# Optimization experiments

Hardware: AMD Instinct MI355X
Metric: run time of the kernel (lower is better)

Reference implementation:

```python
import jax, jax.numpy as jnp
import numpy as np

B, Q, HID = 2, 1024, 2048
NH, NKV, HD = 32, 8, 64          # num heads, kv heads, head_dim (HID = NH*HD)
GROUPS = NH // NKV
KB_N, TOPK = 512, 100            # kb entries, top_k_kb
KB_MAX_TRAIN = 512               # kb_max_train_triples (kb_length_scaling=True)
ROPE_THETA = 10000.0


def rotate_half(x):
    x1, x2 = jnp.split(x, 2, axis=-1)
    return jnp.concatenate([-x2, x1], axis=-1)


def setup_inputs() -> dict:
    key = jax.random.key(0)
    ks = jax.random.split(key, 10)
    sc = 1.0 / np.sqrt(HID)
    hidden_states = jax.random.normal(ks[0], (B, Q, HID), jnp.float32)
    kb_kvs = jax.random.normal(ks[1], (B, KB_N, HID), jnp.float32)
    Wq = jax.random.normal(ks[2], (HID, NH * HD), jnp.float32) * sc
    Wk = jax.random.normal(ks[3], (HID, NKV * HD), jnp.float32) * sc
    Wv = jax.random.normal(ks[4], (HID, NKV * HD), jnp.float32) * sc
    Wo = jax.random.normal(ks[5], (NH * HD, HID), jnp.float32) * sc
    Wq_new = jax.random.normal(ks[6], (HID, NH * HD), jnp.float32) * sc
    Wkb_k = jax.random.normal(ks[7], (HID, NKV * HD), jnp.float32) * sc
    Wkb_v = jax.random.normal(ks[8], (HID, NKV * HD), jnp.float32) * sc
    # RoPE tables [Q, HD]
    inv_freq = 1.0 / (ROPE_THETA ** (jnp.arange(0, HD, 2, dtype=jnp.float32) / HD))
    t = jnp.arange(Q, dtype=jnp.float32)
    freqs = t[:, None] * inv_freq[None, :]
    emb = jnp.concatenate([freqs, freqs], axis=-1)
    cos, sin = jnp.cos(emb), jnp.sin(emb)
    position_ids = jnp.broadcast_to(jnp.arange(Q), (B, Q))
    # additive causal mask [B,1,Q,Q]
    i = jnp.arange(Q)
    causal = jnp.where(i[None, :] <= i[:, None], 0.0, -1e9).astype(jnp.float32)
    attention_mask = jnp.broadcast_to(causal[None, None], (B, 1, Q, Q))
    return dict(hidden_states=hidden_states, kb_kvs=kb_kvs, Wq=Wq, Wk=Wk, Wv=Wv,
                Wo=Wo, Wq_new=Wq_new, Wkb_k=Wkb_k, Wkb_v=Wkb_v, cos=cos, sin=sin,
                attention_mask=attention_mask, position_ids=position_ids)


def attention_fwd(hidden_states, kb_kvs, Wq, Wk, Wv, Wo, Wq_new, Wkb_k, Wkb_v,
                  cos, sin, attention_mask, position_ids):
    b, q_len, _ = hidden_states.shape
    q = (hidden_states @ Wq).reshape(b, q_len, NH, HD).transpose(0, 2, 1, 3)
    k = (hidden_states @ Wk).reshape(b, q_len, NKV, HD).transpose(0, 2, 1, 3)
    v = (hidden_states @ Wv).reshape(b, q_len, NKV, HD).transpose(0, 2, 1, 3)
    # RoPE
    c = cos[position_ids][:, None]  # [b,1,q,hd]
    s = sin[position_ids][:, None]
    q = q * c + rotate_half(q) * s
    k = k * c + rotate_half(k) * s
    # repeat_kv (GQA expansion)
    k = jnp.repeat(k, GROUPS, axis=1)
    v = jnp.repeat(v, GROUPS, axis=1)
    # KB branch (layer_idx=0, kb_layer_index=0 -> slice is full hidden dim)
    kb_k = (kb_kvs @ Wkb_k).reshape(b, KB_N, NKV, HD).transpose(0, 2, 1, 3)
    kb_v = (kb_kvs @ Wkb_v).reshape(b, KB_N, NKV, HD).transpose(0, 2, 1, 3)
    kb_k = jnp.repeat(kb_k, GROUPS, axis=1)
    kb_v = jnp.repeat(kb_v, GROUPS, axis=1)
    kb_q = (hidden_states @ Wq_new).reshape(b, q_len, NH, HD).transpose(0, 2, 1, 3)
    scale = 1.0 / jnp.sqrt(jnp.float32(HD))
    aw_kb = jnp.einsum('bhqd,bhkd->bhqk', kb_q, kb_k) * scale  # [b,nh,q,KB_N]
    # top-k KB entry selection (scores summed over heads and query positions)
    sel_scores = aw_kb.sum(axis=(1, 2))                        # [b,KB_N]
    _, top_idx = jax.lax.top_k(sel_scores, TOPK)               # [b,TOPK]
    kb_v = jnp.take_along_axis(kb_v, top_idx[:, None, :, None], axis=2)
    aw_kb = jnp.take_along_axis(aw_kb, top_idx[:, None, None, :], axis=3)
    # kb length scaling: log(max_train_triples) - log(current kb len)
    aw_kb = aw_kb + (jnp.log(jnp.float32(KB_MAX_TRAIN)) - jnp.log(jnp.float32(TOPK)))
    aw_p = jnp.einsum('bhqd,bhkd->bhqk', q, k) * scale + attention_mask
    aw = jax.nn.softmax(jnp.concatenate([aw_kb, aw_p], axis=-1).astype(jnp.float32), axis=-1)
    aw = aw.astype(q.dtype)
    cv = jnp.concatenate([kb_v, v], axis=2)                    # [b,nh,TOPK+q,hd]
    out = jnp.einsum('bhqk,bhkd->bhqd', aw, cv)
    out = out.transpose(0, 2, 1, 3).reshape(b, q_len, NH * HD)
    return out @ Wo


def reference(hidden_states, kb_kvs, Wq, Wk, Wv, Wo, Wq_new, Wkb_k, Wkb_v,
              cos, sin, attention_mask, position_ids):
    return attention_fwd(hidden_states, kb_kvs, Wq, Wk, Wv, Wo, Wq_new, Wkb_k,
                         Wkb_v, cos, sin, attention_mask, position_ids)
```

## Files before the change

kernel.cpp:

```cpp
#include <hip/hip_runtime.h>

typedef unsigned short u16;
typedef unsigned int   u32;
typedef __bf16 bf16_t;
typedef bf16_t bf16x8 __attribute__((ext_vector_type(8)));
typedef float  floatx4 __attribute__((ext_vector_type(4)));

#define B_    2
#define QS    1024
#define HID_  2048
#define NH_   32
#define NKV_  8
#define HD_   64
#define KBN_  512
#define TOPK_ 100
#define FS    5120

__device__ __forceinline__ float b2f(u16 u) {
  union { u32 i; float f; } x; x.i = ((u32)u) << 16; return x.f;
}
__device__ __forceinline__ u16 f2b(float f) {
  union { float f; u32 i; } x; x.f = f;
  u32 r = x.i + 0x7fffu + ((x.i >> 16) & 1u);
  return (u16)(r >> 16);
}
__device__ __forceinline__ void async16(const u16* g, u16* l) {
  __builtin_amdgcn_global_load_lds(
      (const __attribute__((address_space(1))) unsigned int*)g,
      (__attribute__((address_space(3))) unsigned int*)l, 16, 0, 0);
}

__global__ __launch_bounds__(256)
void cast_f2b(const float* __restrict__ x, u16* __restrict__ y, int n4) {
  int i = blockIdx.x * 256 + threadIdx.x;
  if (i >= n4) return;
  float4 v = ((const float4*)x)[i];
  ((uint2*)y)[i] = make_uint2((u32)f2b(v.x) | ((u32)f2b(v.y) << 16),
                              (u32)f2b(v.z) | ((u32)f2b(v.w) << 16));
}

__global__ __launch_bounds__(256)
void transpose_cast_k(const float* __restrict__ W, u16* __restrict__ WT, int K, int N) {
  __shared__ float tile[32][33];
  int n0 = blockIdx.x * 32, k0 = blockIdx.y * 32;
  int tx = threadIdx.x & 31, ty = threadIdx.x >> 5;
#pragma unroll
  for (int i = 0; i < 32; i += 8)
    tile[ty + i][tx] = W[(size_t)(k0 + ty + i) * N + n0 + tx];
  __syncthreads();
#pragma unroll
  for (int i = 0; i < 32; i += 8)
    WT[(size_t)(n0 + ty + i) * K + k0 + tx] = f2b(tile[tx][ty + i]);
}

__global__ __launch_bounds__(512, 2)
void gemm256(const u16* __restrict__ A, const u16* __restrict__ BT,
             u16* __restrict__ C, int M, int N, int K, int CS) {
  (void)M;
  __shared__ __align__(16) u16 sm[65536];
  const int tid = threadIdx.x, lane = tid & 63, w = tid >> 6;
  const int wr = w >> 2, wc = w & 3;
  const int nbx = N >> 8;
  int nwg = gridDim.x, orig = blockIdx.x, swz = orig;
  if ((nwg & 7) == 0) swz = (orig & 7) * (nwg >> 3) + (orig >> 3);
  int bx = swz % nbx, by = swz / nbx;
  int m0 = by << 8, n0 = bx << 8;
  const int NT = K >> 6;

  int lr = lane >> 2;
  int colsw = ((lane & 3) * 8) ^ ((lane & 32) ? 16 : 0);
  const u16* gA[2][2]; const u16* gB[2][2];
  int lA[2][2];
#pragma unroll
  for (int h = 0; h < 2; ++h)
#pragma unroll
    for (int j = 0; j < 2; ++j) {
      int ij = 2 * w + j, kk = ij >> 3, rb = (ij & 7) * 16;
      gA[h][j] = A + (size_t)(m0 + h * 128 + rb + lr) * K + kk * 32 + colsw;
      gB[h][j] = BT + (size_t)(n0 + h * 128 + rb + lr) * K + kk * 32 + colsw;
      lA[h][j] = kk * 8192 + (h * 128 + rb) * 32;
    }
  int fsw = ((lane >> 4) * 8) ^ ((lane & 8) ? 16 : 0);
  int aoff = (wr * 128 + (lane & 15)) * 32 + fsw;
  int boff = 16384 + (wc * 64 + (lane & 15)) * 32 + fsw;

  floatx4 acc[8][4];
#pragma unroll
  for (int i = 0; i < 8; ++i)
#pragma unroll
    for (int j = 0; j < 4; ++j) acc[i][j] = (floatx4){0.f, 0.f, 0.f, 0.f};
  bf16x8 a[4][2], b[4][2];

#define STG_(g, l, u) async16((g) + (size_t)(u) * 64, &sm[(((u) & 1) << 15) + (l)])
#define BAR_ do { asm volatile("" ::: "memory"); __builtin_amdgcn_s_barrier(); \
                  asm volatile("" ::: "memory"); } while (0)
#define LG0_ do { asm volatile("s_waitcnt lgkmcnt(0)" ::: "memory"); \
                  __builtin_amdgcn_sched_barrier(0); } while (0)

  STG_(gA[0][0], lA[0][0], 0); STG_(gA[0][1], lA[0][1], 0);
  STG_(gA[1][0], lA[1][0], 0); STG_(gA[1][1], lA[1][1], 0);
  STG_(gB[0][0], lA[0][0] + 16384, 0); STG_(gB[0][1], lA[0][1] + 16384, 0);
  STG_(gB[1][0], lA[1][0] + 16384, 0); STG_(gB[1][1], lA[1][1] + 16384, 0);
  if (NT > 1) {
    STG_(gB[0][0], lA[0][0] + 16384, 1); STG_(gB[0][1], lA[0][1] + 16384, 1);
    STG_(gA[0][0], lA[0][0], 1); STG_(gA[0][1], lA[0][1], 1);
    asm volatile("s_waitcnt vmcnt(4)" ::: "memory");
  } else {
    asm volatile("s_waitcnt vmcnt(0)" ::: "memory");
  }
  BAR_;

  for (int u = 0; u < NT; ++u) {
    const int cb = (u & 1) << 15;
#pragma unroll
    for (int kk = 0; kk < 2; ++kk) {
#pragma unroll
      for (int mi = 0; mi < 4; ++mi)
        a[mi][kk] = *(const bf16x8*)&sm[cb + kk * 8192 + aoff + mi * 512];
#pragma unroll
      for (int ni = 0; ni < 2; ++ni)
        b[ni][kk] = *(const bf16x8*)&sm[cb + kk * 8192 + boff + ni * 512];
    }
    if (u + 1 < NT) { STG_(gA[1][0], lA[1][0], u + 1); STG_(gA[1][1], lA[1][1], u + 1); }
    BAR_; LG0_;
    __builtin_amdgcn_s_setprio(1);
#pragma unroll
    for (int mi = 0; mi < 4; ++mi)
#pragma unroll
      for (int ni = 0; ni < 2; ++ni)
#pragma unroll
        for (int kk = 0; kk < 2; ++kk)
          acc[mi][ni] = __builtin_amdgcn_mfma_f32_16x16x32_bf16(
              a[mi][kk], b[ni][kk], acc[mi][ni], 0, 0, 0);
    __builtin_amdgcn_s_setprio(0);
    BAR_;
#pragma unroll
    for (int kk = 0; kk < 2; ++kk)
#pragma unroll
      for (int ni = 0; ni < 2; ++ni)
        b[2 + ni][kk] = *(const bf16x8*)&sm[cb + kk * 8192 + boff + (2 + ni) * 512];
    if (u + 1 < NT) { STG_(gB[1][0], lA[1][0] + 16384, u + 1);
                      STG_(gB[1][1], lA[1][1] + 16384, u + 1); }
    BAR_; LG0_;
    __builtin_amdgcn_s_setprio(1);
#pragma unroll
    for (int mi = 0; mi < 4; ++mi)
#pragma unroll
      for (int ni = 0; ni < 2; ++ni)
#pragma unroll
        for (int kk = 0; kk < 2; ++kk)
          acc[mi][2 + ni] = __builtin_amdgcn_mfma_f32_16x16x32_bf16(
              a[mi][kk], b[2 + ni][kk], acc[mi][2 + ni], 0, 0, 0);
    __builtin_amdgcn_s_setprio(0);
    BAR_;
#pragma unroll
    for (int kk = 0; kk < 2; ++kk)
#pragma unroll
      for (int mi = 0; mi < 4; ++mi)
        a[mi][kk] = *(const bf16x8*)&sm[cb + kk * 8192 + aoff + 2048 + mi * 512];
    if (u + 2 < NT) { STG_(gB[0][0], lA[0][0] + 16384, u + 2);
                      STG_(gB[0][1], lA[0][1] + 16384, u + 2); }
    BAR_; LG0_;
    __builtin_amdgcn_s_setprio(1);
#pragma unroll
    for (int mi = 0; mi < 4; ++mi)
#pragma unroll
      for (int ni = 0; ni < 2; ++ni)
#pragma unroll
        for (int kk = 0; kk < 2; ++kk)
          acc[4 + mi][2 + ni] = __builtin_amdgcn_mfma_f32_16x16x32_bf16(
              a[mi][kk], b[2 + ni][kk], acc[4 + mi][2 + ni], 0, 0, 0);
    __builtin_amdgcn_s_setprio(0);
    BAR_;
    if (u + 2 < NT) {
      STG_(gA[0][0], lA[0][0], u + 2); STG_(gA[0][1], lA[0][1], u + 2);
      asm volatile("s_waitcnt vmcnt(4)" ::: "memory");
    } else {
      asm volatile("s_waitcnt vmcnt(0)" ::: "memory");
    }
    BAR_;
    __builtin_amdgcn_s_setprio(1);
#pragma unroll
    for (int mi = 0; mi < 4; ++mi)
#pragma unroll
      for (int ni = 0; ni < 2; ++ni)
#pragma unroll
        for (int kk = 0; kk < 2; ++kk)
          acc[4 + mi][ni] = __builtin_amdgcn_mfma_f32_16x16x32_bf16(
              a[mi][kk], b[ni][kk], acc[4 + mi][ni], 0, 0, 0);
    __builtin_amdgcn_s_setprio(0);
    BAR_;
  }
#undef STG_
#undef BAR_
#undef LG0_
  int quad = lane >> 4, col = lane & 15;
#pragma unroll
  for (int mi = 0; mi < 8; ++mi)
#pragma unroll
    for (int ni = 0; ni < 4; ++ni)
#pragma unroll
      for (int rr = 0; rr < 4; ++rr)
        C[(size_t)(m0 + wr * 128 + mi * 16 + quad * 4 + rr) * CS +
          n0 + wc * 64 + ni * 16 + col] = f2b(acc[mi][ni][rr]);
}

__global__ __launch_bounds__(512, 2)
void gemm256s(const u16* __restrict__ A, const u16* __restrict__ BT,
              float* __restrict__ P, int N, int LDK, int Kl, int ntiles) {
  __shared__ __align__(16) u16 sm[65536];
  const int tid = threadIdx.x, lane = tid & 63, w = tid >> 6;
  const int wr = w >> 2, wc = w & 3;
  const int nbx = N >> 8;
  int nwg = gridDim.x, orig = blockIdx.x, swz = orig;
  if ((nwg & 7) == 0) swz = (orig & 7) * (nwg >> 3) + (orig >> 3);
  int tile = swz % ntiles, slice = swz / ntiles;
  int bx = tile % nbx, by = tile / nbx;
  int m0 = by << 8, n0 = bx << 8;
  const int NT = Kl >> 6;
  const u16* As = A + (size_t)slice * Kl;
  const u16* Bs = BT + (size_t)slice * Kl;

  int lr = lane >> 2;
  int colsw = ((lane & 3) * 8) ^ ((lane & 32) ? 16 : 0);
  const u16* gA[2][2]; const u16* gB[2][2];
  int lA[2][2];
#pragma unroll
  for (int h = 0; h < 2; ++h)
#pragma unroll
    for (int j = 0; j < 2; ++j) {
      int ij = 2 * w + j, kk = ij >> 3, rb = (ij & 7) * 16;
      gA[h][j] = As + (size_t)(m0 + h * 128 + rb + lr) * LDK + kk * 32 + colsw;
      gB[h][j] = Bs + (size_t)(n0 + h * 128 + rb + lr) * LDK + kk * 32 + colsw;
      lA[h][j] = kk * 8192 + (h * 128 + rb) * 32;
    }
  int fsw = ((lane >> 4) * 8) ^ ((lane & 8) ? 16 : 0);
  int aoff = (wr * 128 + (lane & 15)) * 32 + fsw;
  int boff = 16384 + (wc * 64 + (lane & 15)) * 32 + fsw;

  floatx4 acc[8][4];
#pragma unroll
  for (int i = 0; i < 8; ++i)
#pragma unroll
    for (int j = 0; j < 4; ++j) acc[i][j] = (floatx4){0.f, 0.f, 0.f, 0.f};
  bf16x8 a[4][2], b[4][2];

#define STG_(g, l, u) async16((g) + (size_t)(u) * 64, &sm[(((u) & 1) << 15) + (l)])
#define BAR_ do { asm volatile("" ::: "memory"); __builtin_amdgcn_s_barrier(); \
                  asm volatile("" ::: "memory"); } while (0)
#define LG0_ do { asm volatile("s_waitcnt lgkmcnt(0)" ::: "memory"); \
                  __builtin_amdgcn_sched_barrier(0); } while (0)

  STG_(gA[0][0], lA[0][0], 0); STG_(gA[0][1], lA[0][1], 0);
  STG_(gA[1][0], lA[1][0], 0); STG_(gA[1][1], lA[1][1], 0);
  STG_(gB[0][0], lA[0][0] + 16384, 0); STG_(gB[0][1], lA[0][1] + 16384, 0);
  STG_(gB[1][0], lA[1][0] + 16384, 0); STG_(gB[1][1], lA[1][1] + 16384, 0);
  if (NT > 1) {
    STG_(gB[0][0], lA[0][0] + 16384, 1); STG_(gB[0][1], lA[0][1] + 16384, 1);
    STG_(gA[0][0], lA[0][0], 1); STG_(gA[0][1], lA[0][1], 1);
    asm volatile("s_waitcnt vmcnt(4)" ::: "memory");
  } else {
    asm volatile("s_waitcnt vmcnt(0)" ::: "memory");
  }
  BAR_;

  for (int u = 0; u < NT; ++u) {
    const int cb = (u & 1) << 15;
#pragma unroll
    for (int kk = 0; kk < 2; ++kk) {
#pragma unroll
      for (int mi = 0; mi < 4; ++mi)
        a[mi][kk] = *(const bf16x8*)&sm[cb + kk * 8192 + aoff + mi * 512];
#pragma unroll
      for (int ni = 0; ni < 2; ++ni)
        b[ni][kk] = *(const bf16x8*)&sm[cb + kk * 8192 + boff + ni * 512];
    }
    if (u + 1 < NT) { STG_(gA[1][0], lA[1][0], u + 1); STG_(gA[1][1], lA[1][1], u + 1); }
    BAR_; LG0_;
    __builtin_amdgcn_s_setprio(1);
#pragma unroll
    for (int mi = 0; mi < 4; ++mi)
#pragma unroll
      for (int ni = 0; ni < 2; ++ni)
#pragma unroll
        for (int kk = 0; kk < 2; ++kk)
          acc[mi][ni] = __builtin_amdgcn_mfma_f32_16x16x32_bf16(
              a[mi][kk], b[ni][kk], acc[mi][ni], 0, 0, 0);
    __builtin_amdgcn_s_setprio(0);
    BAR_;
#pragma unroll
    for (int kk = 0; kk < 2; ++kk)
#pragma unroll
      for (int ni = 0; ni < 2; ++ni)
        b[2 + ni][kk] = *(const bf16x8*)&sm[cb + kk * 8192 + boff + (2 + ni) * 512];
    if (u + 1 < NT) { STG_(gB[1][0], lA[1][0] + 16384, u + 1);
                      STG_(gB[1][1], lA[1][1] + 16384, u + 1); }
    BAR_; LG0_;
    __builtin_amdgcn_s_setprio(1);
#pragma unroll
    for (int mi = 0; mi < 4; ++mi)
#pragma unroll
      for (int ni = 0; ni < 2; ++ni)
#pragma unroll
        for (int kk = 0; kk < 2; ++kk)
          acc[mi][2 + ni] = __builtin_amdgcn_mfma_f32_16x16x32_bf16(
              a[mi][kk], b[2 + ni][kk], acc[mi][2 + ni], 0, 0, 0);
    __builtin_amdgcn_s_setprio(0);
    BAR_;
#pragma unroll
    for (int kk = 0; kk < 2; ++kk)
#pragma unroll
      for (int mi = 0; mi < 4; ++mi)
        a[mi][kk] = *(const bf16x8*)&sm[cb + kk * 8192 + aoff + 2048 + mi * 512];
    if (u + 2 < NT) { STG_(gB[0][0], lA[0][0] + 16384, u + 2);
                      STG_(gB[0][1], lA[0][1] + 16384, u + 2); }
    BAR_; LG0_;
    __builtin_amdgcn_s_setprio(1);
#pragma unroll
    for (int mi = 0; mi < 4; ++mi)
#pragma unroll
      for (int ni = 0; ni < 2; ++ni)
#pragma unroll
        for (int kk = 0; kk < 2; ++kk)
          acc[4 + mi][2 + ni] = __builtin_amdgcn_mfma_f32_16x16x32_bf16(
              a[mi][kk], b[2 + ni][kk], acc[4 + mi][2 + ni], 0, 0, 0);
    __builtin_amdgcn_s_setprio(0);
    BAR_;
    if (u + 2 < NT) {
      STG_(gA[0][0], lA[0][0], u + 2); STG_(gA[0][1], lA[0][1], u + 2);
      asm volatile("s_waitcnt vmcnt(4)" ::: "memory");
    } else {
      asm volatile("s_waitcnt vmcnt(0)" ::: "memory");
    }
    BAR_;
    __builtin_amdgcn_s_setprio(1);
#pragma unroll
    for (int mi = 0; mi < 4; ++mi)
#pragma unroll
      for (int ni = 0; ni < 2; ++ni)
#pragma unroll
        for (int kk = 0; kk < 2; ++kk)
          acc[4 + mi][ni] = __builtin_amdgcn_mfma_f32_16x16x32_bf16(
              a[mi][kk], b[ni][kk], acc[4 + mi][ni], 0, 0, 0);
    __builtin_amdgcn_s_setprio(0);
    BAR_;
  }
#undef STG_
#undef BAR_
#undef LG0_
  int quad = lane >> 4, col = lane & 15;
  float* Pp = P + (size_t)slice * ((size_t)ntiles << 16);
#pragma unroll
  for (int mi = 0; mi < 8; ++mi)
#pragma unroll
    for (int ni = 0; ni < 4; ++ni)
#pragma unroll
      for (int rr = 0; rr < 4; ++rr)
        Pp[(size_t)(m0 + wr * 128 + mi * 16 + quad * 4 + rr) * N +
           n0 + wc * 64 + ni * 16 + col] = acc[mi][ni][rr];
}

template <bool TOB16>
__global__ __launch_bounds__(256)
void redp_k(const float* __restrict__ P, void* __restrict__ out, int nslice, int len4) {
  int i = blockIdx.x * 256 + threadIdx.x;
  if (i >= len4) return;
  float4 a = ((const float4*)P)[i];
  for (int s = 1; s < nslice; ++s) {
    float4 b = ((const float4*)P)[(size_t)s * len4 + i];
    a.x += b.x; a.y += b.y; a.z += b.z; a.w += b.w;
  }
  if constexpr (TOB16)
    ((uint2*)out)[i] = make_uint2((u32)f2b(a.x) | ((u32)f2b(a.y) << 16),
                                  (u32)f2b(a.z) | ((u32)f2b(a.w) << 16));
  else
    ((float4*)out)[i] = a;
}

__global__ __launch_bounds__(256)
void rope_k(u16* __restrict__ x, int rs, const float* __restrict__ ct,
            const float* __restrict__ st, const int* __restrict__ pid, int nh, int total) {
  int gid = blockIdx.x * 256 + threadIdx.x;
  if (gid >= total) return;
  int per_row = nh * 32;
  int row = gid / per_row;
  int rem = gid - row * per_row;
  int h = rem >> 5, d = rem & 31;
  int pos = pid[row];
  float c = ct[pos * 64 + d];
  float s = st[pos * 64 + d];
  size_t base = (size_t)row * rs + h * 64 + d;
  float x0 = b2f(x[base]), x1 = b2f(x[base + 32]);
  x[base]      = f2b(x0 * c - x1 * s);
  x[base + 32] = f2b(x1 * c + x0 * s);
}

__global__ __launch_bounds__(256)
void red_d_k(const double* __restrict__ part, double* __restrict__ out, int nchunk, int len) {
  int i = blockIdx.x * 256 + threadIdx.x;
  if (i >= len) return;
  double a = 0.0;
  for (int c = 0; c < nchunk; ++c) a += part[(size_t)c * len + i];
  out[i] = a;
}

__global__ __launch_bounds__(256)
void hssum_part_k(const float* __restrict__ hs, double* __restrict__ part) {
  int qc = blockIdx.x, b = blockIdx.y, t = threadIdx.x;
  double a[8] = {0, 0, 0, 0, 0, 0, 0, 0};
  for (int qq = 0; qq < 16; ++qq) {
    const float* row = hs + (size_t)(b * QS + qc * 16 + qq) * HID_;
#pragma unroll
    for (int m = 0; m < 8; ++m) a[m] += (double)row[m * 256 + t];
  }
#pragma unroll
  for (int m = 0; m < 8; ++m)
    part[(size_t)qc * (B_ * HID_) + b * HID_ + m * 256 + t] = a[m];
}

__global__ __launch_bounds__(512)
void selS_part_k(const double* __restrict__ hssum, const float* __restrict__ Wqn,
                 double* __restrict__ part) {
  int chunk = blockIdx.x, b = blockIdx.y, j = threadIdx.x;
  int g = j >> 6, d = j & 63;
  int c0 = chunk * 16;
  double acc = 0.0;
  for (int cc = 0; cc < 16; ++cc) {
    int c = c0 + cc;
    const float* w = Wqn + (size_t)c * HID_ + g * 256 + d;
    acc += hssum[b * HID_ + c] *
           ((double)w[0] + (double)w[64] + (double)w[128] + (double)w[192]);
  }
  part[(size_t)chunk * (B_ * 512) + b * 512 + j] = acc;
}

__global__ __launch_bounds__(256)
void selU_part_k(const double* __restrict__ S, const float* __restrict__ Wkbk,
                 double* __restrict__ part) {
  int jc = blockIdx.x;
  int b = blockIdx.y >> 3;
  int c = (blockIdx.y & 7) * 256 + threadIdx.x;
  const float* row = Wkbk + (size_t)c * 512 + jc * 128;
  const double* Sp = S + b * 512 + jc * 128;
  double acc = 0.0;
  for (int j = 0; j < 128; j += 4) {
    float4 wv = *(const float4*)(row + j);
    acc += Sp[j] * (double)wv.x + Sp[j + 1] * (double)wv.y +
           Sp[j + 2] * (double)wv.z + Sp[j + 3] * (double)wv.w;
  }
  part[(size_t)jc * (B_ * HID_) + b * HID_ + c] = acc;
}

__global__ __launch_bounds__(256)
void self_part_k(const double* __restrict__ U, const float* __restrict__ kbin,
                 double* __restrict__ part) {
  int n = blockIdx.x * 256 + threadIdx.x;
  int cc = blockIdx.y, b = blockIdx.z;
  const float* row = kbin + (size_t)(b * KBN_ + n) * HID_ + cc * 256;
  const double* u = U + b * HID_ + cc * 256;
  double acc = 0.0;
  for (int c = 0; c < 256; c += 4) {
    float4 kv = *(const float4*)(row + c);
    acc += u[c] * (double)kv.x + u[c + 1] * (double)kv.y +
           u[c + 2] * (double)kv.z + u[c + 3] * (double)kv.w;
  }
  part[(size_t)cc * (B_ * KBN_) + b * KBN_ + n] = acc;
}

__global__ __launch_bounds__(512)
void topk_rank_k(const double* __restrict__ partSel, int* __restrict__ idx) {
  int b = blockIdx.x, i = threadIdx.x;
  __shared__ float v[KBN_];
  double a = 0.0;
#pragma unroll
  for (int c = 0; c < 8; ++c) a += partSel[(size_t)c * (B_ * KBN_) + b * KBN_ + i];
  float vi = (float)a;
  v[i] = vi;
  __syncthreads();
  int rank = 0;
#pragma unroll 8
  for (int j = 0; j < KBN_; ++j) {
    float vj = v[j];
    rank += (vj > vi || (vj == vi && j < i)) ? 1 : 0;
  }
  if (rank < TOPK_) idx[b * TOPK_ + rank] = i;
}

__global__ __launch_bounds__(256)
void vtrans_k(const u16* __restrict__ fused, u16* __restrict__ vt) {
  int kt = blockIdx.x;
  int bg = blockIdx.y;
  int b = bg >> 3, g = bg & 7;
  int t = threadIdx.x;
  __shared__ u16 tile[64][72];
  {
    int kk = t >> 2, dc = (t & 3) * 16;
    const u16* src = fused + (size_t)(b * QS + kt * 64 + kk) * FS + 2560 + g * 64 + dc;
    *(uint4*)&tile[kk][dc]     = *(const uint4*)src;
    *(uint4*)&tile[kk][dc + 8] = *(const uint4*)(src + 8);
  }
  __syncthreads();
  {
    int d = t >> 2, kc = t & 3;
    __align__(16) u16 tmp[16];
#pragma unroll
    for (int i = 0; i < 16; ++i) tmp[i] = tile[kc * 16 + i][d];
    u16* dst = vt + ((size_t)bg * 64 + d) * 1024 + kt * 64 + kc * 16;
    *(uint4*)dst       = *(uint4*)&tmp[0];
    *(uint4*)(dst + 8) = *(uint4*)&tmp[8];
  }
}

__global__ __launch_bounds__(256)
void kbgather_k(const u16* __restrict__ kbf, const int* __restrict__ topidx,
                u16* __restrict__ kbt) {
  int bg = blockIdx.x; int b = bg >> 3, g = bg & 7;
  int t = threadIdx.x;
  int d = t >> 2, s0 = (t & 3) * 32;
  __align__(16) u16 tmp[32];
#pragma unroll
  for (int i = 0; i < 32; ++i) {
    int slot = s0 + i;
    int n = topidx[b * TOPK_ + (slot < TOPK_ ? slot : TOPK_ - 1)];
    tmp[i] = kbf[(size_t)(b * KBN_ + n) * 1024 + 512 + g * 64 + d];
  }
  u16* dst = kbt + ((size_t)bg * 64 + d) * 128 + s0;
#pragma unroll
  for (int i = 0; i < 32; i += 8) *(uint4*)(dst + i) = *(uint4*)&tmp[i];
}

__global__ __launch_bounds__(256)
void attn_mfma_k(const u16* __restrict__ fused, const u16* __restrict__ kbf,
                 const u16* __restrict__ vt, const u16* __restrict__ kbt,
                 const int* __restrict__ topidx, u16* __restrict__ ctx) {
  int bid = blockIdx.x;
  int raw = bid >> 6;
  int hb = bid & 63;
  int h = hb & 31, b = hb >> 5;
  int pg = raw >> 2, pp = raw & 3;
  int pbase = (pg >> 1) * 4 + pp;
  int qt = (pg & 1) ? (15 - pbase) : pbase;
  int g = h >> 2;
  int t = threadIdx.x, lane = t & 63, w = t >> 6;
  int quad = lane >> 4, col = lane & 15;
  __shared__ __align__(16) u16 ks[64 * 72];
  __shared__ __align__(16) u16 vst[64 * 64];
  __shared__ __align__(16) u16 ps[4][16 * 72];
  const float LOGADJ = 1.6331544f;
  int q0 = qt * 64;

  int qrow_frag = q0 + w * 16 + col;
  bf16x8 aKB[2], aC[2];
#pragma unroll
  for (int kstep = 0; kstep < 2; ++kstep) {
    const u16* p1 = fused + (size_t)(b * QS + qrow_frag) * FS + 3072 + h * 64 + kstep * 32 + quad * 8;
    const u16* p2 = fused + (size_t)(b * QS + qrow_frag) * FS + 0    + h * 64 + kstep * 32 + quad * 8;
    uint4 x1 = *(const uint4*)p1, x2 = *(const uint4*)p2;
    const u16* u1 = (const u16*)&x1; const u16* u2 = (const u16*)&x2;
#pragma unroll
    for (int i = 0; i < 8; ++i) {
      aKB[kstep][i] = (bf16_t)(0.125f * b2f(u1[i]));
      aC[kstep][i]  = (bf16_t)(0.125f * b2f(u2[i]));
    }
  }

  float mrow[4] = {-1e30f, -1e30f, -1e30f, -1e30f};
  float lrow[4] = {0.f, 0.f, 0.f, 0.f};
  floatx4 acc[4];
#pragma unroll
  for (int nb = 0; nb < 4; ++nb) acc[nb] = (floatx4){0.f, 0.f, 0.f, 0.f};

  int sj = t >> 2, sdc = (t & 3) * 16, sc4 = t & 3;
  uint4 kr0, kr1, vr0, vr1;

#define LOADTILE(TT) do {                                                      \
    int _t = (TT);                                                             \
    const u16 *_src, *_vsrc;                                                   \
    if (_t < 2) {                                                              \
      int _slot = _t * 64 + sj;                                                \
      int _n = topidx[b * TOPK_ + (_slot < TOPK_ ? _slot : TOPK_ - 1)];        \
      _src = kbf + (size_t)(b * KBN_ + _n) * 1024 + g * 64 + sdc;              \
      _vsrc = kbt + ((size_t)(b * 8 + g) * 64 + sj) * 128 + _t * 64 + sc4 * 16;\
    } else {                                                                   \
      int _key = (_t - 2) * 64 + sj;                                           \
      _src = fused + (size_t)(b * QS + _key) * FS + 2048 + g * 64 + sdc;       \
      _vsrc = vt + ((size_t)(b * 8 + g) * 64 + sj) * 1024 + (_t - 2) * 64 + sc4 * 16; \
    }                                                                          \
    kr0 = *(const uint4*)_src;  kr1 = *(const uint4*)(_src + 8);               \
    vr0 = *(const uint4*)_vsrc; vr1 = *(const uint4*)(_vsrc + 8);              \
  } while (0)

  int ntiles = 2 + (q0 >> 6) + 1;
  LOADTILE(0);
  for (int tile = 0; tile < ntiles; ++tile) {
    __syncthreads();
    *(uint4*)&ks[sj * 72 + sdc]     = kr0;
    *(uint4*)&ks[sj * 72 + sdc + 8] = kr1;
    {
      int sw = sj & 7;
      *(uint4*)&vst[sj * 64 + ((2 * sc4)     ^ sw) * 8] = vr0;
      *(uint4*)&vst[sj * 64 + ((2 * sc4 + 1) ^ sw) * 8] = vr1;
    }
    if (tile + 1 < ntiles) LOADTILE(tile + 1);
    __syncthreads();

    bf16x8 aq0 = (tile < 2) ? aKB[0] : aC[0];
    bf16x8 aq1 = (tile < 2) ? aKB[1] : aC[1];
    floatx4 s[4];
#pragma unroll
    for (int nb = 0; nb < 4; ++nb) {
      s[nb] = (floatx4){0.f, 0.f, 0.f, 0.f};
      bf16x8 b0 = *(bf16x8*)&ks[(nb * 16 + col) * 72 + quad * 8];
      bf16x8 b1 = *(bf16x8*)&ks[(nb * 16 + col) * 72 + 32 + quad * 8];
      s[nb] = __builtin_amdgcn_mfma_f32_16x16x32_bf16(aq0, b0, s[nb], 0, 0, 0);
      s[nb] = __builtin_amdgcn_mfma_f32_16x16x32_bf16(aq1, b1, s[nb], 0, 0, 0);
    }
    if (tile < 2) {
      if (tile == 0) {
#pragma unroll
        for (int nb = 0; nb < 4; ++nb)
#pragma unroll
          for (int rr = 0; rr < 4; ++rr) s[nb][rr] += LOGADJ;
      } else {
#pragma unroll
        for (int nb = 0; nb < 4; ++nb) {
          bool dead = (64 + nb * 16 + col) >= TOPK_;
#pragma unroll
          for (int rr = 0; rr < 4; ++rr)
            s[nb][rr] = dead ? -1e30f : (s[nb][rr] + LOGADJ);
        }
      }
    } else if (tile == ntiles - 1) {
      int kbase = (tile - 2) * 64;
#pragma unroll
      for (int nb = 0; nb < 4; ++nb) {
        int key = kbase + nb * 16 + col;
#pragma unroll
        for (int rr = 0; rr < 4; ++rr) {
          int qrow = q0 + w * 16 + quad * 4 + rr;
          if (key > qrow) s[nb][rr] = -1e30f;
        }
      }
    }
    float tm[4];
#pragma unroll
    for (int rr = 0; rr < 4; ++rr)
      tm[rr] = fmaxf(fmaxf(s[0][rr], s[1][rr]), fmaxf(s[2][rr], s[3][rr]));
#pragma unroll
    for (int off = 1; off < 16; off <<= 1)
#pragma unroll
      for (int rr = 0; rr < 4; ++rr)
        tm[rr] = fmaxf(tm[rr], __shfl_xor(tm[rr], off));
    float alpha[4], rs[4];
#pragma unroll
    for (int rr = 0; rr < 4; ++rr) {
      float mn = fmaxf(mrow[rr], tm[rr]);
      alpha[rr] = __expf(mrow[rr] - mn);
      mrow[rr] = mn;
      rs[rr] = 0.f;
    }
#pragma unroll
    for (int nb = 0; nb < 4; ++nb)
#pragma unroll
      for (int rr = 0; rr < 4; ++rr) {
        float ev = __expf(s[nb][rr] - mrow[rr]);
        rs[rr] += ev;
        ps[w][(quad * 4 + rr) * 72 + nb * 16 + col] = f2b(ev);
      }
#pragma unroll
    for (int off = 1; off < 16; off <<= 1)
#pragma unroll
      for (int rr = 0; rr < 4; ++rr)
        rs[rr] += __shfl_xor(rs[rr], off);
#pragma unroll
    for (int rr = 0; rr < 4; ++rr) lrow[rr] = lrow[rr] * alpha[rr] + rs[rr];
#pragma unroll
    for (int nb = 0; nb < 4; ++nb)
#pragma unroll
      for (int rr = 0; rr < 4; ++rr) acc[nb][rr] *= alpha[rr];

    bf16x8 pa0 = *(bf16x8*)&ps[w][col * 72 + quad * 8];
    bf16x8 pa1 = *(bf16x8*)&ps[w][col * 72 + 32 + quad * 8];
#pragma unroll
    for (int nb = 0; nb < 4; ++nb) {
      int d = nb * 16 + col;
      int sw = (d & 7) << 3;
      bf16x8 vb0 = *(bf16x8*)&vst[d * 64 + ((quad * 8) ^ sw)];
      bf16x8 vb1 = *(bf16x8*)&vst[d * 64 + ((32 + quad * 8) ^ sw)];
      acc[nb] = __builtin_amdgcn_mfma_f32_16x16x32_bf16(pa0, vb0, acc[nb], 0, 0, 0);
      acc[nb] = __builtin_amdgcn_mfma_f32_16x16x32_bf16(pa1, vb1, acc[nb], 0, 0, 0);
    }
  }
#undef LOADTILE
#pragma unroll
  for (int rr = 0; rr < 4; ++rr) {
    float inv = 1.f / lrow[rr];
    int qrow = q0 + w * 16 + quad * 4 + rr;
    size_t base = (size_t)(b * QS + qrow) * HID_ + h * 64;
#pragma unroll
    for (int nb = 0; nb < 4; ++nb)
      ctx[base + nb * 16 + col] = f2b(acc[nb][rr] * inv);
  }
}

extern "C" void kernel_launch(void* const* d_in, const int* in_sizes, int n_in,
                              void* d_out, int out_size, void* d_ws, size_t ws_size,
                              hipStream_t stream) {
  (void)in_sizes; (void)n_in; (void)out_size; (void)ws_size;
  const float* hs_f = (const float*)d_in[0];
  const float* kb_f = (const float*)d_in[1];
  const float* Wq   = (const float*)d_in[2];
  const float* Wk   = (const float*)d_in[3];
  const float* Wv   = (const float*)d_in[4];
  const float* Wo   = (const float*)d_in[5];
  const float* Wqn  = (const float*)d_in[6];
  const float* Wkbk = (const float*)d_in[7];
  const float* Wkbv = (const float*)d_in[8];
  const float* cosT = (const float*)d_in[9];
  const float* sinT = (const float*)d_in[10];
  const int*   pid  = (const int*)d_in[12];
  float* out = (float*)d_out;

  char* p = (char*)d_ws;
  u16* WT    = (u16*)p; p += (size_t)FS * 2048 * 2;
  u16* fused = (u16*)p; p += (size_t)B_ * QS * FS * 2;
  u16* hs_b  = (u16*)p; p += (size_t)B_ * QS * HID_ * 2;
  u16* kb_b  = (u16*)p; p += (size_t)B_ * KBN_ * HID_ * 2;
  u16* kbf   = (u16*)p; p += (size_t)B_ * KBN_ * 1024 * 2;
  double* hssum_ws = (double*)p; p += (size_t)B_ * HID_ * 8;
  double* S_ws     = (double*)p; p += (size_t)B_ * 512 * 8;
  double* U_ws     = (double*)p; p += (size_t)B_ * HID_ * 8;
  float*  sel_ws   = (float*)p;  p += (size_t)B_ * KBN_ * 4;
  int*    idx_ws   = (int*)p;    p += (size_t)B_ * TOPK_ * 4 + 4;
  double* partH    = (double*)p; p += (size_t)64 * B_ * HID_ * 8;
  double* partS    = (double*)p; p += (size_t)128 * B_ * 512 * 8;
  double* partU    = (double*)p; p += (size_t)4 * B_ * HID_ * 8;
  double* partSel  = (double*)p; p += (size_t)8 * B_ * KBN_ * 8;
  float*  partKG   = (float*)p;  p += (size_t)8 * 1024 * 1024 * 4;
  u16* ctx_ws = hs_b;
  u16* v_t    = kb_b;
  u16* kb_t   = kb_b + (size_t)B_ * 8 * 64 * 1024;

  dim3 blk(256);
  cast_f2b<<<dim3((B_ * QS * HID_ / 4 + 255) / 256), blk, 0, stream>>>(hs_f, hs_b, B_ * QS * HID_ / 4);
  cast_f2b<<<dim3((B_ * KBN_ * HID_ / 4 + 255) / 256), blk, 0, stream>>>(kb_f, kb_b, B_ * KBN_ * HID_ / 4);
  transpose_cast_k<<<dim3(64, 64), blk, 0, stream>>>(Wq,  WT,                        2048, 2048);
  transpose_cast_k<<<dim3(16, 64), blk, 0, stream>>>(Wk,  WT + (size_t)2048 * 2048, 2048, 512);
  transpose_cast_k<<<dim3(16, 64), blk, 0, stream>>>(Wv,  WT + (size_t)2560 * 2048, 2048, 512);
  transpose_cast_k<<<dim3(64, 64), blk, 0, stream>>>(Wqn, WT + (size_t)3072 * 2048, 2048, 2048);
  gemm256<<<dim3((FS / 256) * (2048 / 256)), dim3(512), 0, stream>>>(
      hs_b, WT, fused, 2048, FS, 2048, FS);
  transpose_cast_k<<<dim3(16, 64), blk, 0, stream>>>(Wkbk, WT,                       2048, 512);
  transpose_cast_k<<<dim3(16, 64), blk, 0, stream>>>(Wkbv, WT + (size_t)512 * 2048,  2048, 512);
  gemm256s<<<dim3(16 * 8), dim3(512), 0, stream>>>(kb_b, WT, partKG, 1024, 2048, 256, 16);
  redp_k<true><<<dim3((1024 * 1024 / 4 + 255) / 256), blk, 0, stream>>>(
      partKG, kbf, 8, 1024 * 1024 / 4);
  rope_k<<<dim3((B_ * QS * NH_ * 32) / 256), blk, 0, stream>>>(fused, FS, cosT, sinT, pid, NH_, B_ * QS * NH_ * 32);
  rope_k<<<dim3((B_ * QS * NKV_ * 32) / 256), blk, 0, stream>>>(fused + 2048, FS, cosT, sinT, pid, NKV_, B_ * QS * NKV_ * 32);
  hssum_part_k<<<dim3(64, B_), blk, 0, stream>>>(hs_f, partH);
  red_d_k<<<dim3((B_ * HID_ + 255) / 256), blk, 0, stream>>>(partH, hssum_ws, 64, B_ * HID_);
  selS_part_k<<<dim3(128, B_), dim3(512), 0, stream>>>(hssum_ws, Wqn, partS);
  red_d_k<<<dim3((B_ * 512 + 255) / 256), blk, 0, stream>>>(partS, S_ws, 128, B_ * 512);
  selU_part_k<<<dim3(4, B_ * 8), blk, 0, stream>>>(S_ws, Wkbk, partU);
  red_d_k<<<dim3((B_ * HID_ + 255) / 256), blk, 0, stream>>>(partU, U_ws, 4, B_ * HID_);
  self_part_k<<<dim3(2, 8, B_), blk, 0, stream>>>(U_ws, kb_f, partSel);
  topk_rank_k<<<dim3(B_), dim3(512), 0, stream>>>(partSel, idx_ws);
  vtrans_k<<<dim3(16, B_ * 8), blk, 0, stream>>>(fused, v_t);
  kbgather_k<<<dim3(B_ * 8), blk, 0, stream>>>(kbf, idx_ws, kb_t);
  attn_mfma_k<<<dim3(16 * NH_ * B_), blk, 0, stream>>>(fused, kbf, v_t, kb_t, idx_ws, ctx_ws);
  transpose_cast_k<<<dim3(64, 64), blk, 0, stream>>>(Wo, WT, 2048, 2048);
  gemm256s<<<dim3(64 * 2), dim3(512), 0, stream>>>(ctx_ws, WT, partKG, 2048, 2048, 1024, 64);
  redp_k<false><<<dim3((2048 * 2048 / 4 + 255) / 256), blk, 0, stream>>>(
      partKG, out, 2, 2048 * 2048 / 4);
}
```

Baseline: 451.9 us.

## Merge cast, weight-transpose, projection GEMM and RoPE launches into joint kernels

Fuses the two input casts into one kernel, the six weight transpose-casts into one grid-partitioned kernel, and the main QKV projection GEMM with the KB key/value projection GEMM into a single 176-block launch. The KB GEMM now runs as full K=2048 tiles writing bf16 directly, replacing the split-K partial plus reduction pass. The two RoPE launches are also merged. The aim is to cut launch overhead and fill the GPU better by co-scheduling the small KB GEMM with the large one, at the cost of a separate weight buffer and hardcoded grid partitioning.

```diff
diff --git a/kernel.cpp b/kernel.cpp
--- a/kernel.cpp
+++ b/kernel.cpp
@@ -31,11 +31,17 @@
 }
 
 __global__ __launch_bounds__(256)
-void cast_f2b(const float* __restrict__ x, u16* __restrict__ y, int n4) {
+void cast2_k(const float* __restrict__ hs, const float* __restrict__ kb,
+             u16* __restrict__ hsb, u16* __restrict__ kbb) {
   int i = blockIdx.x * 256 + threadIdx.x;
-  if (i >= n4) return;
-  float4 v = ((const float4*)x)[i];
-  ((uint2*)y)[i] = make_uint2((u32)f2b(v.x) | ((u32)f2b(v.y) << 16),
+  const int n1 = B_ * QS * HID_ / 4;
+  const int n2 = B_ * KBN_ * HID_ / 4;
+  const float* x; u16* y; int j;
+  if (i < n1)            { x = hs; y = hsb; j = i; }
+  else if (i < n1 + n2)  { x = kb; y = kbb; j = i - n1; }
+  else return;
+  float4 v = ((const float4*)x)[j];
+  ((uint2*)y)[j] = make_uint2((u32)f2b(v.x) | ((u32)f2b(v.y) << 16),
                               (u32)f2b(v.z) | ((u32)f2b(v.w) << 16));
 }
 
@@ -53,17 +59,44 @@
     WT[(size_t)(n0 + ty + i) * K + k0 + tx] = f2b(tile[tx][ty + i]);
 }
 
+__global__ __launch_bounds__(256)
+void tc6_k(const float* __restrict__ Wq, const float* __restrict__ Wk,
+           const float* __restrict__ Wv, const float* __restrict__ Wqn,
+           const float* __restrict__ Wkbk, const float* __restrict__ Wkbv,
+           u16* __restrict__ WT, u16* __restrict__ WTkb) {
+  int id = blockIdx.x;
+  const float* W; u16* D; int N, bx, by;
+  if (id < 4096)       { W = Wq;   D = WT;                        N = 2048; int l = id;         bx = l & 63; by = l >> 6; }
+  else if (id < 5120)  { W = Wk;   D = WT + (size_t)2048 * 2048;  N = 512;  int l = id - 4096;  bx = l & 15; by = l >> 4; }
+  else if (id < 6144)  { W = Wv;   D = WT + (size_t)2560 * 2048;  N = 512;  int l = id - 5120;  bx = l & 15; by = l >> 4; }
+  else if (id < 10240) { W = Wqn;  D = WT + (size_t)3072 * 2048;  N = 2048; int l = id - 6144;  bx = l & 63; by = l >> 6; }
+  else if (id < 11264) { W = Wkbk; D = WTkb;                      N = 512;  int l = id - 10240; bx = l & 15; by = l >> 4; }
+  else                 { W = Wkbv; D = WTkb + (size_t)512 * 2048; N = 512;  int l = id - 11264; bx = l & 15; by = l >> 4; }
+  const int K = 2048;
+  __shared__ float tile[32][33];
+  int n0 = bx * 32, k0 = by * 32;
+  int tx = threadIdx.x & 31, ty = threadIdx.x >> 5;
+#pragma unroll
+  for (int i = 0; i < 32; i += 8)
+    tile[ty + i][tx] = W[(size_t)(k0 + ty + i) * N + n0 + tx];
+  __syncthreads();
+#pragma unroll
+  for (int i = 0; i < 32; i += 8)
+    D[(size_t)(n0 + ty + i) * K + k0 + tx] = f2b(tile[tx][ty + i]);
+}
+
 __global__ __launch_bounds__(512, 2)
-void gemm256(const u16* __restrict__ A, const u16* __restrict__ BT,
-             u16* __restrict__ C, int M, int N, int K, int CS) {
-  (void)M;
+void gemm256j(const u16* __restrict__ A0, const u16* __restrict__ B0,
+              u16* __restrict__ C0, const u16* __restrict__ A1,
+              const u16* __restrict__ B1, u16* __restrict__ C1, int K) {
   __shared__ __align__(16) u16 sm[65536];
   const int tid = threadIdx.x, lane = tid & 63, w = tid >> 6;
   const int wr = w >> 2, wc = w & 3;
-  const int nbx = N >> 8;
-  int nwg = gridDim.x, orig = blockIdx.x, swz = orig;
-  if ((nwg & 7) == 0) swz = (orig & 7) * (nwg >> 3) + (orig >> 3);
-  int bx = swz % nbx, by = swz / nbx;
+  int orig = blockIdx.x;
+  int swz = (orig & 7) * 22 + (orig >> 3);
+  const u16 *A, *BT; u16* C; int CS, bx, by;
+  if (swz < 160) { A = A0; BT = B0; C = C0; CS = FS;   bx = swz % 20; by = swz / 20; }
+  else { int t2 = swz - 160; A = A1; BT = B1; C = C1; CS = 1024; bx = t2 & 3; by = t2 >> 2; }
   int m0 = by << 8, n0 = bx << 8;
   const int NT = K >> 6;
 
@@ -378,18 +411,21 @@
 }
 
 __global__ __launch_bounds__(256)
-void rope_k(u16* __restrict__ x, int rs, const float* __restrict__ ct,
-            const float* __restrict__ st, const int* __restrict__ pid, int nh, int total) {
+void rope2_k(u16* __restrict__ fused, const float* __restrict__ ct,
+             const float* __restrict__ st, const int* __restrict__ pid) {
   int gid = blockIdx.x * 256 + threadIdx.x;
-  if (gid >= total) return;
+  const int nq = B_ * QS * NH_ * 32;
+  u16* x; int nh, g2;
+  if (gid < nq) { x = fused;        nh = NH_;  g2 = gid; }
+  else          { x = fused + 2048; nh = NKV_; g2 = gid - nq; }
   int per_row = nh * 32;
-  int row = gid / per_row;
-  int rem = gid - row * per_row;
+  int row = g2 / per_row;
+  int rem = g2 - row * per_row;
   int h = rem >> 5, d = rem & 31;
   int pos = pid[row];
   float c = ct[pos * 64 + d];
   float s = st[pos * 64 + d];
-  size_t base = (size_t)row * rs + h * 64 + d;
+  size_t base = (size_t)row * FS + h * 64 + d;
   float x0 = b2f(x[base]), x1 = b2f(x[base + 32]);
   x[base]      = f2b(x0 * c - x1 * s);
   x[base + 32] = f2b(x1 * c + x0 * s);
@@ -723,6 +759,7 @@
 
   char* p = (char*)d_ws;
   u16* WT    = (u16*)p; p += (size_t)FS * 2048 * 2;
+  u16* WTkb  = (u16*)p; p += (size_t)1024 * 2048 * 2;
   u16* fused = (u16*)p; p += (size_t)B_ * QS * FS * 2;
   u16* hs_b  = (u16*)p; p += (size_t)B_ * QS * HID_ * 2;
   u16* kb_b  = (u16*)p; p += (size_t)B_ * KBN_ * HID_ * 2;
@@ -730,7 +767,6 @@
   double* hssum_ws = (double*)p; p += (size_t)B_ * HID_ * 8;
   double* S_ws     = (double*)p; p += (size_t)B_ * 512 * 8;
   double* U_ws     = (double*)p; p += (size_t)B_ * HID_ * 8;
-  float*  sel_ws   = (float*)p;  p += (size_t)B_ * KBN_ * 4;
   int*    idx_ws   = (int*)p;    p += (size_t)B_ * TOPK_ * 4 + 4;
   double* partH    = (double*)p; p += (size_t)64 * B_ * HID_ * 8;
   double* partS    = (double*)p; p += (size_t)128 * B_ * 512 * 8;
@@ -742,21 +778,12 @@
   u16* kb_t   = kb_b + (size_t)B_ * 8 * 64 * 1024;
 
   dim3 blk(256);
-  cast_f2b<<<dim3((B_ * QS * HID_ / 4 + 255) / 256), blk, 0, stream>>>(hs_f, hs_b, B_ * QS * HID_ / 4);
-  cast_f2b<<<dim3((B_ * KBN_ * HID_ / 4 + 255) / 256), blk, 0, stream>>>(kb_f, kb_b, B_ * KBN_ * HID_ / 4);
-  transpose_cast_k<<<dim3(64, 64), blk, 0, stream>>>(Wq,  WT,                        2048, 2048);
-  transpose_cast_k<<<dim3(16, 64), blk, 0, stream>>>(Wk,  WT + (size_t)2048 * 2048, 2048, 512);
-  transpose_cast_k<<<dim3(16, 64), blk, 0, stream>>>(Wv,  WT + (size_t)2560 * 2048, 2048, 512);
-  transpose_cast_k<<<dim3(64, 64), blk, 0, stream>>>(Wqn, WT + (size_t)3072 * 2048, 2048, 2048);
-  gemm256<<<dim3((FS / 256) * (2048 / 256)), dim3(512), 0, stream>>>(
-      hs_b, WT, fused, 2048, FS, 2048, FS);
-  transpose_cast_k<<<dim3(16, 64), blk, 0, stream>>>(Wkbk, WT,                       2048, 512);
-  transpose_cast_k<<<dim3(16, 64), blk, 0, stream>>>(Wkbv, WT + (size_t)512 * 2048,  2048, 512);
-  gemm256s<<<dim3(16 * 8), dim3(512), 0, stream>>>(kb_b, WT, partKG, 1024, 2048, 256, 16);
-  redp_k<true><<<dim3((1024 * 1024 / 4 + 255) / 256), blk, 0, stream>>>(
-      partKG, kbf, 8, 1024 * 1024 / 4);
-  rope_k<<<dim3((B_ * QS * NH_ * 32) / 256), blk, 0, stream>>>(fused, FS, cosT, sinT, pid, NH_, B_ * QS * NH_ * 32);
-  rope_k<<<dim3((B_ * QS * NKV_ * 32) / 256), blk, 0, stream>>>(fused + 2048, FS, cosT, sinT, pid, NKV_, B_ * QS * NKV_ * 32);
+  cast2_k<<<dim3((B_ * QS * HID_ / 4 + B_ * KBN_ * HID_ / 4) / 256), blk, 0, stream>>>(
+      hs_f, kb_f, hs_b, kb_b);
+  tc6_k<<<dim3(12288), blk, 0, stream>>>(Wq, Wk, Wv, Wqn, Wkbk, Wkbv, WT, WTkb);
+  gemm256j<<<dim3(176), dim3(512), 0, stream>>>(hs_b, WT, fused, kb_b, WTkb, kbf, 2048);
+  rope2_k<<<dim3((B_ * QS * NH_ * 32 + B_ * QS * NKV_ * 32) / 256), blk, 0, stream>>>(
+      fused, cosT, sinT, pid);
   hssum_part_k<<<dim3(64, B_), blk, 0, stream>>>(hs_f, partH);
   red_d_k<<<dim3((B_ * HID_ + 255) / 256), blk, 0, stream>>>(partH, hssum_ws, 64, B_ * HID_);
   selS_part_k<<<dim3(128, B_), dim3(512), 0, stream>>>(hssum_ws, Wqn, partS);
```

Measured after the change: 413.2 us. -8.6%, faster.
